# Kernel optimization log

Hardware: AMD Instinct MI355X
Metric: run time of the kernel (lower is better)

Reference implementation:

```python
import jax, jax.numpy as jnp
import numpy as np

K_SIZE = 5


def extract_patches(x, k):
    # TF extract_image_patches with SAME zero padding, stride 1.
    # x: [B,H,W,C] -> [B,H,W,k*k,C], patch index ordered row-major over offsets.
    pad = k // 2
    B, H, W, C = x.shape
    xp = jnp.pad(x, ((0, 0), (pad, pad), (pad, pad), (0, 0)))
    slices = [xp[:, i:i + H, j:j + W, :] for i in range(k) for j in range(k)]
    return jnp.stack(slices, axis=3)  # [B,H,W,k*k,C]


def setup_inputs() -> dict:
    key = jax.random.key(0)
    k1, k2, k3, k4 = jax.random.split(key, 4)
    B, H, W, C, BIN = 4, 128, 128, 64, 64
    return {
        "main": jax.random.normal(k1, (B, H, W, C), jnp.float32),
        "main_value": jax.random.normal(k2, (B, H, W, BIN), jnp.float32),
        "ref": jax.random.normal(k3, (B, H, W, C), jnp.float32),
        "ref_value": jax.random.normal(k4, (B, H, W, BIN), jnp.float32),
    }


def reference(main, main_value, ref, ref_value):
    k = K_SIZE
    # local window keys: [B,H,W,k*k,C], then append main itself -> k*k+1 slots
    ref_stacked = extract_patches(ref, k)
    ref_main = jnp.concatenate([ref_stacked, main[:, :, :, None, :]], axis=-2)
    attn = jnp.einsum('bhwc,bhwkc->bhwk', main, ref_main)
    attn = jax.nn.softmax(attn, axis=-1)
    # values: [B,H,W,k*k+1,bin]
    ref_value_stacked = extract_patches(ref_value, k)
    ref_main_value = jnp.concatenate(
        [ref_value_stacked, main_value[:, :, :, None, :]], axis=-2)
    aggregation = jnp.einsum('bhwk,bhwki->bhwi', attn, ref_main_value)
    return aggregation
```

## Files before the change

kernel.cpp:

```cpp
#include <hip/hip_runtime.h>

#define BATCH 4
#define HH 128
#define WW 128
#define CC 64
#define TH 8
#define TW 8
#define HALO 12
#define HPOS 144
#define ROWDW 32
#define KVDW (HPOS*ROWDW)

__device__ __forceinline__ unsigned pack2bf(float a, float b){
  unsigned ua = __float_as_uint(a), ub = __float_as_uint(b);
  ua = (ua + 0x7fffu + ((ua>>16)&1u)) >> 16;
  ub = (ub + 0x7fffu + ((ub>>16)&1u)) >> 16;
  return ua | (ub<<16);
}

__device__ __forceinline__ void unpack8(uint4 u, float* f){
  f[0]=__uint_as_float(u.x<<16); f[1]=__uint_as_float(u.x&0xffff0000u);
  f[2]=__uint_as_float(u.y<<16); f[3]=__uint_as_float(u.y&0xffff0000u);
  f[4]=__uint_as_float(u.z<<16); f[5]=__uint_as_float(u.z&0xffff0000u);
  f[6]=__uint_as_float(u.w<<16); f[7]=__uint_as_float(u.w&0xffff0000u);
}

template<int CTRL>
__device__ __forceinline__ float dpp_addstep(float x){
  int p = __builtin_amdgcn_update_dpp(0, __float_as_int(x), CTRL, 0xf, 0xf, true);
  return x + __int_as_float(p);
}
__device__ __forceinline__ float reduce8(float x){
  x = dpp_addstep<0xB1>(x);
  x = dpp_addstep<0x4E>(x);
  x = dpp_addstep<0x141>(x);
  return x;
}

__global__ __launch_bounds__(256, 2) void local_attn_kernel(
    const float* __restrict__ main_,
    const float* __restrict__ main_value,
    const float* __restrict__ ref,
    const float* __restrict__ ref_value,
    float* __restrict__ out)
{
    __shared__ unsigned kv[2*KVDW];

    const int t   = threadIdx.x;
    const int nwg = BATCH*16*16;
    const int blk = (blockIdx.x & 7) * (nwg>>3) + (blockIdx.x >> 3);
    const int bx  = blk & 15;
    const int by  = (blk>>4) & 15;
    const int b   = blk >> 8;

    const int lane = t & 63;
    const int wave = t >> 6;
    const int cg8  = lane & 7;
    const int lx   = lane >> 3;
    const int ly0  = wave*2;

    const int gx  = bx*TW + lx;
    const int gy0 = by*TH + ly0;

    const size_t img  = (size_t)b*HH*WW*CC;
    const size_t off0 = img + ((size_t)gy0*WW + gx)*CC + cg8*8;
    const size_t off1 = off0 + (size_t)WW*CC;

    float4 qa0 = *(const float4*)(main_+off0), qb0 = *(const float4*)(main_+off0+4);
    float4 qa1 = *(const float4*)(main_+off1), qb1 = *(const float4*)(main_+off1+4);

    const int y0 = by*TH - 2, x0 = bx*TW - 2;

    #pragma unroll
    for (int half = 0; half < 2; ++half) {
        const float* src = half ? ref_value : ref;
        unsigned* dst = kv + half*KVDW;
        #pragma unroll
        for (int it = 0; it < 5; ++it) {
            int u = t + (it<<8);
            if (u < HPOS*8) {
                int pos = u >> 3, c8 = u & 7;
                int hy = pos/12, hx = pos - hy*12;
                int yy = y0+hy, xx = x0+hx;
                float4 a = make_float4(0.f,0.f,0.f,0.f);
                float4 c = make_float4(0.f,0.f,0.f,0.f);
                if ((unsigned)yy < HH && (unsigned)xx < WW) {
                    const float* g = src + img + ((size_t)yy*WW+xx)*CC + c8*8;
                    a = ((const float4*)g)[0];
                    c = ((const float4*)g)[1];
                }
                uint4 w;
                w.x = pack2bf(a.x,a.y); w.y = pack2bf(a.z,a.w);
                w.z = pack2bf(c.x,c.y); w.w = pack2bf(c.z,c.w);
                *(uint4*)(dst + pos*ROWDW + c8*4) = w;
            }
        }
    }

    __syncthreads();

    float4 va0 = *(const float4*)(main_value+off0), vb0 = *(const float4*)(main_value+off0+4);
    float4 va1 = *(const float4*)(main_value+off1), vb1 = *(const float4*)(main_value+off1+4);

    float q0[8] = {qa0.x,qa0.y,qa0.z,qa0.w,qb0.x,qb0.y,qb0.z,qb0.w};
    float q1[8] = {qa1.x,qa1.y,qa1.z,qa1.w,qb1.x,qb1.y,qb1.z,qb1.w};

    float o0[8], o1[8];
    #pragma unroll
    for (int c = 0; c < 8; ++c) { o0[c]=0.f; o1[c]=0.f; }
    float m0 = -INFINITY, m1 = -INFINITY, s0 = 0.f, s1 = 0.f;

    const unsigned* KB = kv;
    const unsigned* VB = kv + KVDW;

    #pragma unroll
    for (int di = 0; di < 6; ++di) {
        #pragma unroll
        for (int dj = 0; dj < 5; ++dj) {
            const int pos = (ly0+di)*HALO + (lx+dj);
            uint4 kk = *(const uint4*)(KB + pos*ROWDW + cg8*4);
            uint4 vv = *(const uint4*)(VB + pos*ROWDW + cg8*4);
            float k[8], v[8];
            unpack8(kk, k);
            unpack8(vv, v);
            if (di < 5) {
                float l = 0.f;
                #pragma unroll
                for (int c = 0; c < 8; ++c) l = fmaf(q0[c], k[c], l);
                l = reduce8(l);
                float mn = fmaxf(m0, l);
                float corr = __expf(m0 - mn);
                float w    = __expf(l  - mn);
                s0 = fmaf(s0, corr, w);
                #pragma unroll
                for (int c = 0; c < 8; ++c) o0[c] = fmaf(o0[c], corr, w * v[c]);
                m0 = mn;
            }
            if (di >= 1) {
                float l = 0.f;
                #pragma unroll
                for (int c = 0; c < 8; ++c) l = fmaf(q1[c], k[c], l);
                l = reduce8(l);
                float mn = fmaxf(m1, l);
                float corr = __expf(m1 - mn);
                float w    = __expf(l  - mn);
                s1 = fmaf(s1, corr, w);
                #pragma unroll
                for (int c = 0; c < 8; ++c) o1[c] = fmaf(o1[c], corr, w * v[c]);
                m1 = mn;
            }
        }
    }

    {
        float mv0[8] = {va0.x,va0.y,va0.z,va0.w,vb0.x,vb0.y,vb0.z,vb0.w};
        float mv1[8] = {va1.x,va1.y,va1.z,va1.w,vb1.x,vb1.y,vb1.z,vb1.w};
        float l0 = 0.f, l1 = 0.f;
        #pragma unroll
        for (int c = 0; c < 8; ++c) { l0 = fmaf(q0[c],q0[c],l0); l1 = fmaf(q1[c],q1[c],l1); }
        l0 = reduce8(l0); l1 = reduce8(l1);
        float mn0 = fmaxf(m0, l0), corr0 = __expf(m0-mn0), w0 = __expf(l0-mn0);
        float mn1 = fmaxf(m1, l1), corr1 = __expf(m1-mn1), w1 = __expf(l1-mn1);
        s0 = fmaf(s0, corr0, w0);
        s1 = fmaf(s1, corr1, w1);
        #pragma unroll
        for (int c = 0; c < 8; ++c) {
            o0[c] = fmaf(o0[c], corr0, w0 * mv0[c]);
            o1[c] = fmaf(o1[c], corr1, w1 * mv1[c]);
        }
    }

    const float rs0 = 1.f/s0, rs1 = 1.f/s1;

    float4 r;
    r.x=o0[0]*rs0; r.y=o0[1]*rs0; r.z=o0[2]*rs0; r.w=o0[3]*rs0;
    *(float4*)(out+off0) = r;
    r.x=o0[4]*rs0; r.y=o0[5]*rs0; r.z=o0[6]*rs0; r.w=o0[7]*rs0;
    *(float4*)(out+off0+4) = r;
    r.x=o1[0]*rs1; r.y=o1[1]*rs1; r.z=o1[2]*rs1; r.w=o1[3]*rs1;
    *(float4*)(out+off1) = r;
    r.x=o1[4]*rs1; r.y=o1[5]*rs1; r.z=o1[6]*rs1; r.w=o1[7]*rs1;
    *(float4*)(out+off1+4) = r;
}

extern "C" void kernel_launch(void* const* d_in, const int* in_sizes, int n_in,
                              void* d_out, int out_size, void* d_ws, size_t ws_size,
                              hipStream_t stream) {
    const float* main_      = (const float*)d_in[0];
    const float* main_value = (const float*)d_in[1];
    const float* ref        = (const float*)d_in[2];
    const float* ref_value  = (const float*)d_in[3];
    float* out = (float*)d_out;

    local_attn_kernel<<<dim3(BATCH*16*16), dim3(256), 0, stream>>>(
        main_, main_value, ref, ref_value, out);
}
```

Baseline: 31.43 us.

## Stream halo rows through double-buffered LDS and use self-score as softmax max

Replaces the single bulk load of the 12x12 K/V halo with a six-stage, two-rows-per-stage double-buffered pipeline, so global loads of the next rows overlap compute on the current ones. LDS shrinks from the full halo to two small buffers with an XOR swizzle to avoid bank conflicts. Pixel-to-wave mapping changes to rows wv and wv+4. The online-softmax max tracking is dropped: the self score |q|^2 is used as a fixed offset. That removes the rescale exps but can overflow if a neighbour score far exceeds |q|^2.

```diff
diff --git a/kernel.cpp b/kernel.cpp
--- a/kernel.cpp
+++ b/kernel.cpp
@@ -1,15 +1,9 @@
 #include <hip/hip_runtime.h>
 
-#define BATCH 4
 #define HH 128
 #define WW 128
 #define CC 64
-#define TH 8
-#define TW 8
-#define HALO 12
-#define HPOS 144
-#define ROWDW 32
-#define KVDW (HPOS*ROWDW)
+#define IMG (HH*WW*CC)
 
 __device__ __forceinline__ unsigned pack2bf(float a, float b){
   unsigned ua = __float_as_uint(a), ub = __float_as_uint(b);
@@ -36,6 +30,27 @@
   x = dpp_addstep<0x141>(x);
   return x;
 }
+
+#define STAGE_LOAD(st, A0,A1,B0,B1) {                                          \
+  A0=A1=B0=B1=make_float4(0.f,0.f,0.f,0.f);                                    \
+  int yya = y0 + 2*(st) + prA;                                                 \
+  if (vxA && (unsigned)yya < HH) {                                             \
+    const float* g = srcA + ((size_t)yya*WW + xxA)*CC + c8s*8;                 \
+    A0 = ((const float4*)g)[0]; A1 = ((const float4*)g)[1];                    \
+  }                                                                            \
+  int yyb = y0 + 2*(st) + prB;                                                 \
+  if (hasB && vxB && (unsigned)yyb < HH) {                                     \
+    const float* g = srcB + ((size_t)yyb*WW + xxB)*CC + c8s*8;                 \
+    B0 = ((const float4*)g)[0]; B1 = ((const float4*)g)[1];                    \
+  } }
+
+#define STAGE_WRITE(bb, A0,A1,B0,B1) {                                         \
+  kv4[(bb)*384 + dstA] = make_uint4(pack2bf(A0.x,A0.y),pack2bf(A0.z,A0.w),     \
+                                    pack2bf(A1.x,A1.y),pack2bf(A1.z,A1.w));    \
+  if (hasB)                                                                    \
+    kv4[(bb)*384 + dstB] = make_uint4(pack2bf(B0.x,B0.y),pack2bf(B0.z,B0.w),   \
+                                      pack2bf(B1.x,B1.y),pack2bf(B1.z,B1.w));  \
+  }
 
 __global__ __launch_bounds__(256, 2) void local_attn_kernel(
     const float* __restrict__ main_,
@@ -44,143 +59,147 @@
     const float* __restrict__ ref_value,
     float* __restrict__ out)
 {
-    __shared__ unsigned kv[2*KVDW];
+    __shared__ uint4 kv4[2*384];
 
     const int t   = threadIdx.x;
-    const int nwg = BATCH*16*16;
-    const int blk = (blockIdx.x & 7) * (nwg>>3) + (blockIdx.x >> 3);
+    const int blk = (blockIdx.x & 7) * 128 + (blockIdx.x >> 3);
     const int bx  = blk & 15;
-    const int by  = (blk>>4) & 15;
+    const int by  = (blk >> 4) & 15;
     const int b   = blk >> 8;
 
     const int lane = t & 63;
-    const int wave = t >> 6;
+    const int wv   = t >> 6;
     const int cg8  = lane & 7;
     const int lx   = lane >> 3;
-    const int ly0  = wave*2;
-
-    const int gx  = bx*TW + lx;
-    const int gy0 = by*TH + ly0;
-
-    const size_t img  = (size_t)b*HH*WW*CC;
-    const size_t off0 = img + ((size_t)gy0*WW + gx)*CC + cg8*8;
-    const size_t off1 = off0 + (size_t)WW*CC;
-
-    float4 qa0 = *(const float4*)(main_+off0), qb0 = *(const float4*)(main_+off0+4);
-    float4 qa1 = *(const float4*)(main_+off1), qb1 = *(const float4*)(main_+off1+4);
-
-    const int y0 = by*TH - 2, x0 = bx*TW - 2;
-
+    const int pya  = wv;
+
+    const int gx = bx*8 + lx;
+    const size_t img  = (size_t)b * IMG;
+    const size_t offA = img + ((size_t)(by*8 + pya)*WW + gx)*CC + cg8*8;
+    const size_t offB = offA + (size_t)4*WW*CC;
+
+    const int y0 = by*8 - 2, x0 = bx*8 - 2;
+
+    float4 qa0 = *(const float4*)(main_+offA), qa1 = *(const float4*)(main_+offA+4);
+    float4 qb0 = *(const float4*)(main_+offB), qb1 = *(const float4*)(main_+offB+4);
+
+    const int   mA  = (t >= 192);
+    const int   rA  = t - 192*mA;
+    const int   posA= rA >> 3;
+    const int   c8s = t & 7;
+    const int   prA = (posA >= 12);
+    const int   pcA = posA - 12*prA;
+    const int   xxA = x0 + pcA;
+    const bool  vxA = (unsigned)xxA < WW;
+    const float* srcA = (mA ? ref_value : ref) + img;
+    const int   dstA = mA*192 + posA*8 + (c8s ^ (posA & 7));
+
+    const bool  hasB = (t < 128);
+    const int   posB = 8 + (t >> 3);
+    const int   prB  = (posB >= 12);
+    const int   pcB  = posB - 12*prB;
+    const int   xxB  = x0 + pcB;
+    const bool  vxB  = (unsigned)xxB < WW;
+    const float* srcB = ref_value + img;
+    const int   dstB = 192 + posB*8 + (c8s ^ (posB & 7));
+
+    {
+        float4 A0,A1,B0,B1;
+        STAGE_LOAD(0, A0,A1,B0,B1);
+        STAGE_WRITE(0, A0,A1,B0,B1);
+    }
+    __syncthreads();
+
+    float qA[8] = {qa0.x,qa0.y,qa0.z,qa0.w,qa1.x,qa1.y,qa1.z,qa1.w};
+    float qB[8] = {qb0.x,qb0.y,qb0.z,qb0.w,qb1.x,qb1.y,qb1.z,qb1.w};
+
+    float lqA, lqB;
+    {
+        float a = 0.f, b2 = 0.f;
+        #pragma unroll
+        for (int c = 0; c < 8; ++c) { a = fmaf(qA[c],qA[c],a); b2 = fmaf(qB[c],qB[c],b2); }
+        lqA = reduce8(a); lqB = reduce8(b2);
+    }
+
+    float oA[8], oB[8];
     #pragma unroll
-    for (int half = 0; half < 2; ++half) {
-        const float* src = half ? ref_value : ref;
-        unsigned* dst = kv + half*KVDW;
+    for (int c = 0; c < 8; ++c) { oA[c]=0.f; oB[c]=0.f; }
+    float sA = 0.f, sB = 0.f;
+
+    #pragma unroll
+    for (int s = 0; s < 6; ++s) {
+        float4 nA0,nA1,nB0,nB1;
+        if (s < 5) STAGE_LOAD(s+1, nA0,nA1,nB0,nB1);
+
+        const int bb = s & 1;
         #pragma unroll
-        for (int it = 0; it < 5; ++it) {
-            int u = t + (it<<8);
-            if (u < HPOS*8) {
-                int pos = u >> 3, c8 = u & 7;
-                int hy = pos/12, hx = pos - hy*12;
-                int yy = y0+hy, xx = x0+hx;
-                float4 a = make_float4(0.f,0.f,0.f,0.f);
-                float4 c = make_float4(0.f,0.f,0.f,0.f);
-                if ((unsigned)yy < HH && (unsigned)xx < WW) {
-                    const float* g = src + img + ((size_t)yy*WW+xx)*CC + c8*8;
-                    a = ((const float4*)g)[0];
-                    c = ((const float4*)g)[1];
+        for (int rl = 0; rl < 2; ++rl) {
+            const int row = 2*s + rl;
+            if (row >= pya && row <= pya+8) {
+                const bool actA = (row <= pya+4);
+                const bool actB = (row >= pya+4);
+                #pragma unroll
+                for (int dj = 0; dj < 5; ++dj) {
+                    const int pl  = rl*12 + lx + dj;
+                    const int sw  = cg8 ^ (pl & 7);
+                    const uint4 kk = kv4[bb*384 +       pl*8 + sw];
+                    const uint4 vv = kv4[bb*384 + 192 + pl*8 + sw];
+                    float k8[8], v8[8];
+                    unpack8(kk, k8);
+                    unpack8(vv, v8);
+                    if (actA) {
+                        float l = 0.f;
+                        #pragma unroll
+                        for (int c = 0; c < 8; ++c) l = fmaf(qA[c], k8[c], l);
+                        l = reduce8(l);
+                        float w = __expf(l - lqA);
+                        sA += w;
+                        #pragma unroll
+                        for (int c = 0; c < 8; ++c) oA[c] = fmaf(w, v8[c], oA[c]);
+                    }
+                    if (actB) {
+                        float l = 0.f;
+                        #pragma unroll
+                        for (int c = 0; c < 8; ++c) l = fmaf(qB[c], k8[c], l);
+                        l = reduce8(l);
+                        float w = __expf(l - lqB);
+                        sB += w;
+                        #pragma unroll
+                        for (int c = 0; c < 8; ++c) oB[c] = fmaf(w, v8[c], oB[c]);
+                    }
                 }
-                uint4 w;
-                w.x = pack2bf(a.x,a.y); w.y = pack2bf(a.z,a.w);
-                w.z = pack2bf(c.x,c.y); w.w = pack2bf(c.z,c.w);
-                *(uint4*)(dst + pos*ROWDW + c8*4) = w;
             }
         }
-    }
-
-    __syncthreads();
-
-    float4 va0 = *(const float4*)(main_value+off0), vb0 = *(const float4*)(main_value+off0+4);
-    float4 va1 = *(const float4*)(main_value+off1), vb1 = *(const float4*)(main_value+off1+4);
-
-    float q0[8] = {qa0.x,qa0.y,qa0.z,qa0.w,qb0.x,qb0.y,qb0.z,qb0.w};
-    float q1[8] = {qa1.x,qa1.y,qa1.z,qa1.w,qb1.x,qb1.y,qb1.z,qb1.w};
-
-    float o0[8], o1[8];
-    #pragma unroll
-    for (int c = 0; c < 8; ++c) { o0[c]=0.f; o1[c]=0.f; }
-    float m0 = -INFINITY, m1 = -INFINITY, s0 = 0.f, s1 = 0.f;
-
-    const unsigned* KB = kv;
-    const unsigned* VB = kv + KVDW;
-
-    #pragma unroll
-    for (int di = 0; di < 6; ++di) {
-        #pragma unroll
-        for (int dj = 0; dj < 5; ++dj) {
-            const int pos = (ly0+di)*HALO + (lx+dj);
-            uint4 kk = *(const uint4*)(KB + pos*ROWDW + cg8*4);
-            uint4 vv = *(const uint4*)(VB + pos*ROWDW + cg8*4);
-            float k[8], v[8];
-            unpack8(kk, k);
-            unpack8(vv, v);
-            if (di < 5) {
-                float l = 0.f;
-                #pragma unroll
-                for (int c = 0; c < 8; ++c) l = fmaf(q0[c], k[c], l);
-                l = reduce8(l);
-                float mn = fmaxf(m0, l);
-                float corr = __expf(m0 - mn);
-                float w    = __expf(l  - mn);
-                s0 = fmaf(s0, corr, w);
-                #pragma unroll
-                for (int c = 0; c < 8; ++c) o0[c] = fmaf(o0[c], corr, w * v[c]);
-                m0 = mn;
-            }
-            if (di >= 1) {
-                float l = 0.f;
-                #pragma unroll
-                for (int c = 0; c < 8; ++c) l = fmaf(q1[c], k[c], l);
-                l = reduce8(l);
-                float mn = fmaxf(m1, l);
-                float corr = __expf(m1 - mn);
-                float w    = __expf(l  - mn);
-                s1 = fmaf(s1, corr, w);
-                #pragma unroll
-                for (int c = 0; c < 8; ++c) o1[c] = fmaf(o1[c], corr, w * v[c]);
-                m1 = mn;
-            }
+
+        if (s < 5) {
+            STAGE_WRITE(bb^1, nA0,nA1,nB0,nB1);
+            __syncthreads();
         }
     }
 
     {
-        float mv0[8] = {va0.x,va0.y,va0.z,va0.w,vb0.x,vb0.y,vb0.z,vb0.w};
-        float mv1[8] = {va1.x,va1.y,va1.z,va1.w,vb1.x,vb1.y,vb1.z,vb1.w};
-        float l0 = 0.f, l1 = 0.f;
-        #pragma unroll
-        for (int c = 0; c < 8; ++c) { l0 = fmaf(q0[c],q0[c],l0); l1 = fmaf(q1[c],q1[c],l1); }
-        l0 = reduce8(l0); l1 = reduce8(l1);
-        float mn0 = fmaxf(m0, l0), corr0 = __expf(m0-mn0), w0 = __expf(l0-mn0);
-        float mn1 = fmaxf(m1, l1), corr1 = __expf(m1-mn1), w1 = __expf(l1-mn1);
-        s0 = fmaf(s0, corr0, w0);
-        s1 = fmaf(s1, corr1, w1);
+        float4 va0 = *(const float4*)(main_value+offA), va1 = *(const float4*)(main_value+offA+4);
+        float4 vb0 = *(const float4*)(main_value+offB), vb1 = *(const float4*)(main_value+offB+4);
+        float mvA[8] = {va0.x,va0.y,va0.z,va0.w,va1.x,va1.y,va1.z,va1.w};
+        float mvB[8] = {vb0.x,vb0.y,vb0.z,vb0.w,vb1.x,vb1.y,vb1.z,vb1.w};
+        sA += 1.f; sB += 1.f;
         #pragma unroll
         for (int c = 0; c < 8; ++c) {
-            o0[c] = fmaf(o0[c], corr0, w0 * mv0[c]);
-            o1[c] = fmaf(o1[c], corr1, w1 * mv1[c]);
+            oA[c] += mvA[c];
+            oB[c] += mvB[c];
         }
     }
 
-    const float rs0 = 1.f/s0, rs1 = 1.f/s1;
-
+    const float rsA = 1.f/sA, rsB = 1.f/sB;
     float4 r;
-    r.x=o0[0]*rs0; r.y=o0[1]*rs0; r.z=o0[2]*rs0; r.w=o0[3]*rs0;
-    *(float4*)(out+off0) = r;
-    r.x=o0[4]*rs0; r.y=o0[5]*rs0; r.z=o0[6]*rs0; r.w=o0[7]*rs0;
-    *(float4*)(out+off0+4) = r;
-    r.x=o1[0]*rs1; r.y=o1[1]*rs1; r.z=o1[2]*rs1; r.w=o1[3]*rs1;
-    *(float4*)(out+off1) = r;
-    r.x=o1[4]*rs1; r.y=o1[5]*rs1; r.z=o1[6]*rs1; r.w=o1[7]*rs1;
-    *(float4*)(out+off1+4) = r;
+    r.x=oA[0]*rsA; r.y=oA[1]*rsA; r.z=oA[2]*rsA; r.w=oA[3]*rsA;
+    *(float4*)(out+offA) = r;
+    r.x=oA[4]*rsA; r.y=oA[5]*rsA; r.z=oA[6]*rsA; r.w=oA[7]*rsA;
+    *(float4*)(out+offA+4) = r;
+    r.x=oB[0]*rsB; r.y=oB[1]*rsB; r.z=oB[2]*rsB; r.w=oB[3]*rsB;
+    *(float4*)(out+offB) = r;
+    r.x=oB[4]*rsB; r.y=oB[5]*rsB; r.z=oB[6]*rsB; r.w=oB[7]*rsB;
+    *(float4*)(out+offB+4) = r;
 }
 
 extern "C" void kernel_launch(void* const* d_in, const int* in_sizes, int n_in,
@@ -192,6 +211,6 @@
     const float* ref_value  = (const float*)d_in[3];
     float* out = (float*)d_out;
 
-    local_attn_kernel<<<dim3(BATCH*16*16), dim3(256), 0, stream>>>(
+    local_attn_kernel<<<dim3(4*16*16), dim3(256), 0, stream>>>(
         main_, main_value, ref, ref_value, out);
 }
```

After: 31.14 us. No clear change (-0.9%).
